# Kernel tuning notes

Hardware: AMD Instinct MI355X
Metric: run time of the kernel (lower is better)

## Reference

```python
import jax, jax.numpy as jnp
import numpy as np

N_NODES = 20000
N_EDGES = 320000
IN_F = 168
HID = 256


def gcn_conv(x, W, b, src, dst, ew, n_nodes):
    """PyG GCNConv: symmetric normalization with self-loops (fill 1.0).
    out = D^-1/2 (A + I) D^-1/2 X W^T + b, aggregated at dst (source_to_target).
    """
    xw = x @ W.T  # [N, F_out]
    # degree at target nodes, including self-loop weight 1.0
    deg = jax.ops.segment_sum(ew, dst, num_segments=n_nodes) + 1.0
    dinv = jnp.where(deg > 0, jax.lax.rsqrt(deg), 0.0)
    norm = dinv[src] * ew * dinv[dst]  # [E]
    agg = jax.ops.segment_sum(norm[:, None] * xw[src], dst, num_segments=n_nodes)
    # self-loop contribution: norm_ii = dinv[i]^2
    out = agg + (dinv * dinv)[:, None] * xw
    return out + b


def setup_inputs() -> dict:
    key = jax.random.key(0)
    k = jax.random.split(key, 8)
    x = jax.random.normal(k[0], (N_NODES, IN_F), dtype=jnp.float32)
    edge_index = jax.random.randint(k[1], (2, N_EDGES), 0, N_NODES, dtype=jnp.int64)
    edge_weight = jax.random.uniform(k[2], (N_EDGES,), dtype=jnp.float32)
    # GCN layer weights (PyG Linear: y = x W^T), plus per-layer bias
    s1 = 1.0 / np.sqrt(IN_F)
    s2 = 1.0 / np.sqrt(HID)
    W1 = jax.random.uniform(k[3], (HID, IN_F), minval=-s1, maxval=s1, dtype=jnp.float32)
    b1 = jnp.zeros((HID,), dtype=jnp.float32)
    W2 = jax.random.uniform(k[4], (HID, HID), minval=-s2, maxval=s2, dtype=jnp.float32)
    b2 = jnp.zeros((HID,), dtype=jnp.float32)
    return {"x": x, "edge_index": edge_index, "edge_weight": edge_weight,
            "W1": W1, "b1": b1, "W2": W2, "b2": b2}


def reference(x, edge_index, edge_weight, W1, b1, W2, b2):
    src, dst = edge_index[0], edge_index[1]
    h = gcn_conv(x, W1, b1, src, dst, edge_weight, N_NODES)
    h = jax.nn.relu(h)
    h = gcn_conv(h, W2, b2, src, dst, edge_weight, N_NODES)
    h = jax.nn.relu(h)
    return h
```

## Files before the change

kernel.cpp:

```cpp
#include <hip/hip_runtime.h>

#define N_NODES 20000
#define N_EDGES 320000
#define IN_F    168
#define HID     256
#define K1P     192
#define XS      192
#define NF4     42
#define X4      48

typedef __attribute__((ext_vector_type(8))) short bf16x8;
typedef __attribute__((ext_vector_type(4))) float f32x4;
typedef __attribute__((ext_vector_type(2))) float f32x2;

__device__ __forceinline__ short f2bf(float f) {
    union { float f; unsigned u; } v; v.f = f;
    unsigned r = v.u + 0x7FFFu + ((v.u >> 16) & 1u);
    return (short)(r >> 16);
}
__device__ __forceinline__ f32x2 bfp(unsigned u) {
    f32x2 r;
    r.x = __uint_as_float(u << 16);
    r.y = __uint_as_float(u & 0xFFFF0000u);
    return r;
}

__global__ void prep_all(const float* __restrict__ x, short* __restrict__ xb,
                         const float* __restrict__ W1, const float* __restrict__ W2,
                         short* __restrict__ w1b, short* __restrict__ w2b,
                         const int* __restrict__ ei, const float* __restrict__ ew,
                         float* __restrict__ deg, int* __restrict__ counts) {
    const int xTot  = N_NODES * X4;
    const int w1Tot = 256 * X4;
    const int w2Tot = 256 * 64;
    int i = blockIdx.x * 256 + threadIdx.x;
    if (i < xTot) {
        int n  = i / X4;
        int k4 = i - n * X4;
        short4 o;
        if (k4 < NF4) {
            float4 v = *(const float4*)(x + (size_t)n * IN_F + k4 * 4);
            o = make_short4(f2bf(v.x), f2bf(v.y), f2bf(v.z), f2bf(v.w));
        } else {
            o = make_short4(0, 0, 0, 0);
        }
        *(short4*)(xb + (size_t)n * XS + k4 * 4) = o;
        return;
    }
    i -= xTot;
    if (i < w1Tot) {
        int r  = i / X4;
        int k4 = i - r * X4;
        short4 o;
        if (k4 < NF4) {
            float4 v = *(const float4*)(W1 + (size_t)r * IN_F + k4 * 4);
            o = make_short4(f2bf(v.x), f2bf(v.y), f2bf(v.z), f2bf(v.w));
        } else {
            o = make_short4(0, 0, 0, 0);
        }
        *(short4*)(w1b + (size_t)r * K1P + k4 * 4) = o;
        return;
    }
    i -= w1Tot;
    if (i < w2Tot) {
        int r  = i >> 6;
        int c4 = i & 63;
        float4 v = *(const float4*)(W2 + (size_t)r * HID + c4 * 4);
        *(short4*)(w2b + (size_t)r * HID + c4 * 4) =
            make_short4(f2bf(v.x), f2bf(v.y), f2bf(v.z), f2bf(v.w));
        return;
    }
    i -= w2Tot;
    if (i < N_EDGES) {
        int d = ei[N_EDGES + i];
        atomicAdd(&deg[d], ew[i]);
        atomicAdd(&counts[d], 1);
    }
}


__global__ __launch_bounds__(1024) void scan_part(const int* __restrict__ counts,
                                                  int* __restrict__ offs,
                                                  int* __restrict__ bsum,
                                                  float* __restrict__ deg, int n) {
    int tid  = threadIdx.x;
    int lane = tid & 63;
    int wv   = tid >> 6;
    int i = blockIdx.x * 1024 + tid;
    if (i < n) deg[i] = rsqrtf(deg[i] + 1.0f);
    __shared__ int wsum[16];
    int v = (i < n) ? ((counts[i] + 7) & ~7) : 0;
    int incl = v;
    #pragma unroll
    for (int d = 1; d < 64; d <<= 1) {
        int t = __shfl_up(incl, d);
        if (lane >= d) incl += t;
    }
    if (lane == 63) wsum[wv] = incl;
    __syncthreads();
    if (wv == 0) {
        int w = (lane < 16) ? wsum[lane] : 0;
        int winc = w;
        #pragma unroll
        for (int d = 1; d < 16; d <<= 1) {
            int t = __shfl_up(winc, d);
            if (lane >= d) winc += t;
        }
        if (lane < 16) wsum[lane] = winc - w;
    }
    __syncthreads();
    if (i < n) offs[i] = wsum[wv] + incl - v;
    if (tid == 1023) bsum[blockIdx.x] = wsum[15] + incl;
}

__global__ __launch_bounds__(1024) void scan_add(const int* __restrict__ bsum,
                                                 int* __restrict__ offs, int n) {
    int i = blockIdx.x * 1024 + threadIdx.x;
    int add = 0;
    for (int b = 0; b < (int)blockIdx.x; ++b) add += bsum[b];
    if (i < n) offs[i] += add;
    if (i == n) offs[n] = add + bsum[blockIdx.x];
}

__global__ void scatter_edges(const int* __restrict__ ei, const float* __restrict__ ew,
                              const float* __restrict__ dinv, const int* __restrict__ offs,
                              const int* __restrict__ counts,
                              int* __restrict__ cursor, int2* __restrict__ er) {
    int t = blockIdx.x * 256 + threadIdx.x;
    if (t < N_EDGES) {
        int s = ei[t];
        int d = ei[N_EDGES + t];
        int pos = offs[d] + atomicAdd(&cursor[d], 1);
        float nm = dinv[s] * ew[t] * dinv[d];
        er[pos] = make_int2(s, __float_as_int(nm));
        return;
    }
    int n = t - N_EDGES;
    if (n < N_NODES) {
        int p   = offs[n] + counts[n];
        int end = offs[n + 1];
        for (; p < end; ++p) er[p] = make_int2(0, 0);
    }
}


__global__ __launch_bounds__(256) void agg_x(const short* __restrict__ xb,
                                             const float* __restrict__ dinv,
                                             const int* __restrict__ offs,
                                             const int2* __restrict__ er,
                                             short* __restrict__ ax) {
    int wave = threadIdx.x >> 6;
    int lane = threadIdx.x & 63;
    int n = blockIdx.x * 4 + wave;
    bool act = lane < NF4;
    int lo4 = act ? lane * 4 : 0;
    float di = dinv[n];
    float sw = di * di;
    uint2 sv = *(const uint2*)(xb + (size_t)n * XS + lo4);
    f32x2 a01 = bfp(sv.x) * sw;
    f32x2 a23 = bfp(sv.y) * sw;

    int p0 = offs[n], p1 = offs[n + 1];
    for (int p = p0; p < p1; p += 8) {
        const int4* e4 = (const int4*)(er + p);
        int4 eA = e4[0], eB = e4[1], eC = e4[2], eD = e4[3];
        uint2 r0 = *(const uint2*)(xb + (size_t)eA.x * XS + lo4);
        uint2 r1 = *(const uint2*)(xb + (size_t)eA.z * XS + lo4);
        uint2 r2 = *(const uint2*)(xb + (size_t)eB.x * XS + lo4);
        uint2 r3 = *(const uint2*)(xb + (size_t)eB.z * XS + lo4);
        uint2 r4 = *(const uint2*)(xb + (size_t)eC.x * XS + lo4);
        uint2 r5 = *(const uint2*)(xb + (size_t)eC.z * XS + lo4);
        uint2 r6 = *(const uint2*)(xb + (size_t)eD.x * XS + lo4);
        uint2 r7 = *(const uint2*)(xb + (size_t)eD.z * XS + lo4);
        float w0 = __int_as_float(eA.y), w1 = __int_as_float(eA.w);
        float w2 = __int_as_float(eB.y), w3 = __int_as_float(eB.w);
        float w4 = __int_as_float(eC.y), w5 = __int_as_float(eC.w);
        float w6 = __int_as_float(eD.y), w7 = __int_as_float(eD.w);
        a01 += bfp(r0.x) * w0; a23 += bfp(r0.y) * w0;
        a01 += bfp(r1.x) * w1; a23 += bfp(r1.y) * w1;
        a01 += bfp(r2.x) * w2; a23 += bfp(r2.y) * w2;
        a01 += bfp(r3.x) * w3; a23 += bfp(r3.y) * w3;
        a01 += bfp(r4.x) * w4; a23 += bfp(r4.y) * w4;
        a01 += bfp(r5.x) * w5; a23 += bfp(r5.y) * w5;
        a01 += bfp(r6.x) * w6; a23 += bfp(r6.y) * w6;
        a01 += bfp(r7.x) * w7; a23 += bfp(r7.y) * w7;
    }

    size_t base = (size_t)n * K1P + lane * 4;
    if (act) {
        *(short4*)&ax[base] = make_short4(f2bf(a01.x), f2bf(a01.y),
                                          f2bf(a23.x), f2bf(a23.y));
    } else if (lane < 48) {
        *(short4*)&ax[base] = make_short4(0, 0, 0, 0);
    }
}

__global__ __launch_bounds__(256) void agg_h(const short* __restrict__ h1h,
                                             const float* __restrict__ dinv,
                                             const int* __restrict__ offs,
                                             const int2* __restrict__ er,
                                             short* __restrict__ ah) {
    int wave = threadIdx.x >> 6;
    int lane = threadIdx.x & 63;
    int n = blockIdx.x * 4 + wave;
    int lo4 = lane * 4;
    float di = dinv[n];
    float sw = di * di;
    uint2 sv = *(const uint2*)(h1h + (size_t)n * HID + lo4);
    f32x2 a01 = bfp(sv.x) * sw;
    f32x2 a23 = bfp(sv.y) * sw;

    int p0 = offs[n], p1 = offs[n + 1];
    for (int p = p0; p < p1; p += 8) {
        const int4* e4 = (const int4*)(er + p);
        int4 eA = e4[0], eB = e4[1], eC = e4[2], eD = e4[3];
        uint2 r0 = *(const uint2*)(h1h + (size_t)eA.x * HID + lo4);
        uint2 r1 = *(const uint2*)(h1h + (size_t)eA.z * HID + lo4);
        uint2 r2 = *(const uint2*)(h1h + (size_t)eB.x * HID + lo4);
        uint2 r3 = *(const uint2*)(h1h + (size_t)eB.z * HID + lo4);
        uint2 r4 = *(const uint2*)(h1h + (size_t)eC.x * HID + lo4);
        uint2 r5 = *(const uint2*)(h1h + (size_t)eC.z * HID + lo4);
        uint2 r6 = *(const uint2*)(h1h + (size_t)eD.x * HID + lo4);
        uint2 r7 = *(const uint2*)(h1h + (size_t)eD.z * HID + lo4);
        float w0 = __int_as_float(eA.y), w1 = __int_as_float(eA.w);
        float w2 = __int_as_float(eB.y), w3 = __int_as_float(eB.w);
        float w4 = __int_as_float(eC.y), w5 = __int_as_float(eC.w);
        float w6 = __int_as_float(eD.y), w7 = __int_as_float(eD.w);
        a01 += bfp(r0.x) * w0; a23 += bfp(r0.y) * w0;
        a01 += bfp(r1.x) * w1; a23 += bfp(r1.y) * w1;
        a01 += bfp(r2.x) * w2; a23 += bfp(r2.y) * w2;
        a01 += bfp(r3.x) * w3; a23 += bfp(r3.y) * w3;
        a01 += bfp(r4.x) * w4; a23 += bfp(r4.y) * w4;
        a01 += bfp(r5.x) * w5; a23 += bfp(r5.y) * w5;
        a01 += bfp(r6.x) * w6; a23 += bfp(r6.y) * w6;
        a01 += bfp(r7.x) * w7; a23 += bfp(r7.y) * w7;
    }

    *(short4*)&ah[(size_t)n * HID + lo4] = make_short4(f2bf(a01.x), f2bf(a01.y),
                                                       f2bf(a23.x), f2bf(a23.y));
}


#define LDS_STRIDE 72

__global__ __launch_bounds__(256) void gemm_bf(const short* __restrict__ Ah,
                                               const short* __restrict__ Wh,
                                               const float* __restrict__ bias,
                                               float* __restrict__ Cf,
                                               short* __restrict__ Cbf,
                                               int M, int Ks, int nsteps, int mode) {
    __shared__ short sAh[64 * LDS_STRIDE];
    __shared__ short sWh[64 * LDS_STRIDE];

    const int idx   = blockIdx.x;
    const int group = idx >> 5;
    const int xcd   = idx & 7;
    const int slot  = (idx >> 3) & 3;
    const int mt    = group * 8 + xcd;
    const int mtiles = (M + 63) >> 6;
    if (mt >= mtiles) return;
    const int bm = mt * 64;
    const int bn = slot * 64;

    const int tid  = threadIdx.x;
    const int lane = tid & 63;
    const int wv   = tid >> 6;
    const int l16  = lane & 15;
    const int quad = lane >> 4;
    const int wm   = (wv & 1) * 32;
    const int wn   = (wv >> 1) * 32;

    const int srow = tid >> 2;
    const int sseg = (tid & 3) * 16;
    int arow = bm + srow; if (arow >= M) arow = M - 1;
    const short* gAh = Ah + (size_t)arow * Ks;
    const short* gWh = Wh + (size_t)(bn + srow) * Ks;
    const int lds_off = srow * LDS_STRIDE + sseg;

    f32x4 acc00 = {0,0,0,0}, acc01 = {0,0,0,0}, acc10 = {0,0,0,0}, acc11 = {0,0,0,0};

    int4 pah0 = *(const int4*)(gAh + sseg), pah1 = *(const int4*)(gAh + sseg + 8);
    int4 pwh0 = *(const int4*)(gWh + sseg), pwh1 = *(const int4*)(gWh + sseg + 8);

    for (int ks = 0; ks < nsteps; ++ks) {
        *(int4*)&sAh[lds_off] = pah0; *(int4*)&sAh[lds_off + 8] = pah1;
        *(int4*)&sWh[lds_off] = pwh0; *(int4*)&sWh[lds_off + 8] = pwh1;
        __syncthreads();
        if (ks + 1 < nsteps) {
            int o = (ks + 1) * 64 + sseg;
            pah0 = *(const int4*)(gAh + o); pah1 = *(const int4*)(gAh + o + 8);
            pwh0 = *(const int4*)(gWh + o); pwh1 = *(const int4*)(gWh + o + 8);
        }
        #pragma unroll
        for (int o = 0; o < 2; ++o) {
            const int a0 = (wm + l16) * LDS_STRIDE + o * 32 + quad * 8;
            const int a1 = a0 + 16 * LDS_STRIDE;
            const int w0 = (wn + l16) * LDS_STRIDE + o * 32 + quad * 8;
            const int w1 = w0 + 16 * LDS_STRIDE;
            bf16x8 ah0 = *(const bf16x8*)&sAh[a0];
            bf16x8 ah1 = *(const bf16x8*)&sAh[a1];
            bf16x8 wh0 = *(const bf16x8*)&sWh[w0];
            bf16x8 wh1 = *(const bf16x8*)&sWh[w1];
            acc00 = __builtin_amdgcn_mfma_f32_16x16x32_bf16(ah0, wh0, acc00, 0, 0, 0);
            acc01 = __builtin_amdgcn_mfma_f32_16x16x32_bf16(ah0, wh1, acc01, 0, 0, 0);
            acc10 = __builtin_amdgcn_mfma_f32_16x16x32_bf16(ah1, wh0, acc10, 0, 0, 0);
            acc11 = __builtin_amdgcn_mfma_f32_16x16x32_bf16(ah1, wh1, acc11, 0, 0, 0);
        }
        __syncthreads();
    }

    const int colb = bn + wn + l16;
    const int rowb = bm + wm + quad * 4;
    const float b0 = bias[colb];
    const float b1 = bias[colb + 16];
    #pragma unroll
    for (int r = 0; r < 4; ++r) {
        int row = rowb + r;
        if (row < M) {
            float v0 = acc00[r] + b0; v0 = v0 > 0.f ? v0 : 0.f;
            float v1 = acc01[r] + b1; v1 = v1 > 0.f ? v1 : 0.f;
            if (mode == 0) {
                Cbf[(size_t)row * HID + colb]      = f2bf(v0);
                Cbf[(size_t)row * HID + colb + 16] = f2bf(v1);
            } else {
                Cf[(size_t)row * HID + colb]      = v0;
                Cf[(size_t)row * HID + colb + 16] = v1;
            }
        }
        int row2 = row + 16;
        if (row2 < M) {
            float v0 = acc10[r] + b0; v0 = v0 > 0.f ? v0 : 0.f;
            float v1 = acc11[r] + b1; v1 = v1 > 0.f ? v1 : 0.f;
            if (mode == 0) {
                Cbf[(size_t)row2 * HID + colb]      = f2bf(v0);
                Cbf[(size_t)row2 * HID + colb + 16] = f2bf(v1);
            } else {
                Cf[(size_t)row2 * HID + colb]      = v0;
                Cf[(size_t)row2 * HID + colb + 16] = v1;
            }
        }
    }
}


extern "C" void kernel_launch(void* const* d_in, const int* in_sizes, int n_in,
                              void* d_out, int out_size, void* d_ws, size_t ws_size,
                              hipStream_t stream) {
    const float* x  = (const float*)d_in[0];
    const int*   ei = (const int*)d_in[1];
    const float* ew = (const float*)d_in[2];
    const float* W1 = (const float*)d_in[3];
    const float* b1 = (const float*)d_in[4];
    const float* W2 = (const float*)d_in[5];
    const float* b2 = (const float*)d_in[6];
    float* out = (float*)d_out;

    char* ws = (char*)d_ws;
    float* deg      = (float*)(ws);
    int*   counts   = (int*)(ws + 80000);
    int*   cursor   = (int*)(ws + 160000);
    int*   offs     = (int*)(ws + 240000);
    int*   bsum     = (int*)(ws + 320016);
    int2*  er       = (int2*)(ws + 320144);
    short* ax       = (short*)(ws + 4160144);
    short* ah       = (short*)(ws + 4160144);
    short* h1h      = (short*)(ws + 14400144);
    short* w1b      = (short*)(ws + 24640144);
    short* w2b      = (short*)(ws + 24738448);
    short* xb       = (short*)(ws + 24869520);

    hipMemsetAsync(d_ws, 0, 320144, stream);

    const int prep_tot = N_NODES * X4 + 256 * X4 + 256 * 64 + N_EDGES;
    prep_all<<<(prep_tot + 255) / 256, 256, 0, stream>>>(
        x, xb, W1, W2, w1b, w2b, ei, ew, deg, counts);
    scan_part<<<20, 1024, 0, stream>>>(counts, offs, bsum, deg, N_NODES);
    scan_add<<<20, 1024, 0, stream>>>(bsum, offs, N_NODES);
    const int sc_blocks = (N_EDGES + N_NODES + 255) / 256;
    scatter_edges<<<sc_blocks, 256, 0, stream>>>(ei, ew, deg, offs, counts, cursor, er);

    const int mtiles = (N_NODES + 63) / 64;
    const int gemm_grid = ((mtiles + 7) / 8) * 32;
    agg_x<<<N_NODES / 4, 256, 0, stream>>>(xb, deg, offs, er, ax);
    gemm_bf<<<gemm_grid, 256, 0, stream>>>(ax, w1b, b1, nullptr, h1h,
                                           N_NODES, K1P, 3, 0);
    agg_h<<<N_NODES / 4, 256, 0, stream>>>(h1h, deg, offs, er, ah);
    gemm_bf<<<gemm_grid, 256, 0, stream>>>(ah, w2b, b2, out, nullptr,
                                           N_NODES, HID, 4, 1);
}
```

Measured before the change: 200.1 us.

## Fuse aggregation with GEMM per layer and merge scan into one kernel

Each layer's neighbor aggregation now writes its 64-row tile straight into shared memory and the same block runs the MFMA GEMM over all four column slots. This removes the global round trip for the aggregated activations and two kernel launches. The two-kernel prefix scan is replaced by a single 1024-thread block in which each thread scans 20 entries. That block also resets the cursor array, so the memset shrinks. The cost is much lower parallelism: only 313 blocks each doing 64 rows of serial gather, plus a single-block scan.

```diff
diff --git a/kernel.cpp b/kernel.cpp
--- a/kernel.cpp
+++ b/kernel.cpp
@@ -8,6 +8,9 @@
 #define XS      192
 #define NF4     42
 #define X4      48
+#define ASTR1   200
+#define ASTR2   264
+#define WSTR    72
 
 typedef __attribute__((ext_vector_type(8))) short bf16x8;
 typedef __attribute__((ext_vector_type(4))) float f32x4;
@@ -78,19 +81,33 @@
     }
 }
 
-
-__global__ __launch_bounds__(1024) void scan_part(const int* __restrict__ counts,
-                                                  int* __restrict__ offs,
-                                                  int* __restrict__ bsum,
-                                                  float* __restrict__ deg, int n) {
-    int tid  = threadIdx.x;
-    int lane = tid & 63;
-    int wv   = tid >> 6;
-    int i = blockIdx.x * 1024 + tid;
-    if (i < n) deg[i] = rsqrtf(deg[i] + 1.0f);
+__global__ __launch_bounds__(1024) void scan1(const int* __restrict__ counts,
+                                              int* __restrict__ offs,
+                                              float* __restrict__ deg,
+                                              int* __restrict__ cursor) {
+    const int tid  = threadIdx.x;
+    const int lane = tid & 63;
+    const int wv   = tid >> 6;
     __shared__ int wsum[16];
-    int v = (i < n) ? ((counts[i] + 7) & ~7) : 0;
-    int incl = v;
+
+    const int base = tid * 20;
+    int loc[20];
+    int s = 0;
+    #pragma unroll
+    for (int j = 0; j < 20; ++j) {
+        int i = base + j;
+        int c = (i < N_NODES) ? ((counts[i] + 7) & ~7) : 0;
+        loc[j] = s; s += c;
+    }
+    #pragma unroll
+    for (int j = 0; j < 20; ++j) {
+        int i = base + j;
+        if (i < N_NODES) {
+            deg[i] = rsqrtf(deg[i] + 1.0f);
+            cursor[i] = 0;
+        }
+    }
+    int incl = s;
     #pragma unroll
     for (int d = 1; d < 64; d <<= 1) {
         int t = __shfl_up(incl, d);
@@ -109,17 +126,13 @@
         if (lane < 16) wsum[lane] = winc - w;
     }
     __syncthreads();
-    if (i < n) offs[i] = wsum[wv] + incl - v;
-    if (tid == 1023) bsum[blockIdx.x] = wsum[15] + incl;
-}
-
-__global__ __launch_bounds__(1024) void scan_add(const int* __restrict__ bsum,
-                                                 int* __restrict__ offs, int n) {
-    int i = blockIdx.x * 1024 + threadIdx.x;
-    int add = 0;
-    for (int b = 0; b < (int)blockIdx.x; ++b) add += bsum[b];
-    if (i < n) offs[i] += add;
-    if (i == n) offs[n] = add + bsum[blockIdx.x];
+    int excl = wsum[wv] + incl - s;
+    #pragma unroll
+    for (int j = 0; j < 20; ++j) {
+        int i = base + j;
+        if (i < N_NODES) offs[i] = excl + loc[j];
+    }
+    if (tid == 1023) offs[N_NODES] = excl + s;
 }
 
 __global__ void scatter_edges(const int* __restrict__ ei, const float* __restrict__ ew,
@@ -143,200 +156,245 @@
     }
 }
 
-
-__global__ __launch_bounds__(256) void agg_x(const short* __restrict__ xb,
-                                             const float* __restrict__ dinv,
-                                             const int* __restrict__ offs,
-                                             const int2* __restrict__ er,
-                                             short* __restrict__ ax) {
-    int wave = threadIdx.x >> 6;
-    int lane = threadIdx.x & 63;
-    int n = blockIdx.x * 4 + wave;
-    bool act = lane < NF4;
-    int lo4 = act ? lane * 4 : 0;
-    float di = dinv[n];
-    float sw = di * di;
-    uint2 sv = *(const uint2*)(xb + (size_t)n * XS + lo4);
-    f32x2 a01 = bfp(sv.x) * sw;
-    f32x2 a23 = bfp(sv.y) * sw;
-
-    int p0 = offs[n], p1 = offs[n + 1];
-    for (int p = p0; p < p1; p += 8) {
-        const int4* e4 = (const int4*)(er + p);
-        int4 eA = e4[0], eB = e4[1], eC = e4[2], eD = e4[3];
-        uint2 r0 = *(const uint2*)(xb + (size_t)eA.x * XS + lo4);
-        uint2 r1 = *(const uint2*)(xb + (size_t)eA.z * XS + lo4);
-        uint2 r2 = *(const uint2*)(xb + (size_t)eB.x * XS + lo4);
-        uint2 r3 = *(const uint2*)(xb + (size_t)eB.z * XS + lo4);
-        uint2 r4 = *(const uint2*)(xb + (size_t)eC.x * XS + lo4);
-        uint2 r5 = *(const uint2*)(xb + (size_t)eC.z * XS + lo4);
-        uint2 r6 = *(const uint2*)(xb + (size_t)eD.x * XS + lo4);
-        uint2 r7 = *(const uint2*)(xb + (size_t)eD.z * XS + lo4);
-        float w0 = __int_as_float(eA.y), w1 = __int_as_float(eA.w);
-        float w2 = __int_as_float(eB.y), w3 = __int_as_float(eB.w);
-        float w4 = __int_as_float(eC.y), w5 = __int_as_float(eC.w);
-        float w6 = __int_as_float(eD.y), w7 = __int_as_float(eD.w);
-        a01 += bfp(r0.x) * w0; a23 += bfp(r0.y) * w0;
-        a01 += bfp(r1.x) * w1; a23 += bfp(r1.y) * w1;
-        a01 += bfp(r2.x) * w2; a23 += bfp(r2.y) * w2;
-        a01 += bfp(r3.x) * w3; a23 += bfp(r3.y) * w3;
-        a01 += bfp(r4.x) * w4; a23 += bfp(r4.y) * w4;
-        a01 += bfp(r5.x) * w5; a23 += bfp(r5.y) * w5;
-        a01 += bfp(r6.x) * w6; a23 += bfp(r6.y) * w6;
-        a01 += bfp(r7.x) * w7; a23 += bfp(r7.y) * w7;
-    }
-
-    size_t base = (size_t)n * K1P + lane * 4;
-    if (act) {
-        *(short4*)&ax[base] = make_short4(f2bf(a01.x), f2bf(a01.y),
-                                          f2bf(a23.x), f2bf(a23.y));
-    } else if (lane < 48) {
-        *(short4*)&ax[base] = make_short4(0, 0, 0, 0);
-    }
-}
-
-__global__ __launch_bounds__(256) void agg_h(const short* __restrict__ h1h,
-                                             const float* __restrict__ dinv,
-                                             const int* __restrict__ offs,
-                                             const int2* __restrict__ er,
-                                             short* __restrict__ ah) {
-    int wave = threadIdx.x >> 6;
-    int lane = threadIdx.x & 63;
-    int n = blockIdx.x * 4 + wave;
-    int lo4 = lane * 4;
-    float di = dinv[n];
-    float sw = di * di;
-    uint2 sv = *(const uint2*)(h1h + (size_t)n * HID + lo4);
-    f32x2 a01 = bfp(sv.x) * sw;
-    f32x2 a23 = bfp(sv.y) * sw;
-
-    int p0 = offs[n], p1 = offs[n + 1];
-    for (int p = p0; p < p1; p += 8) {
-        const int4* e4 = (const int4*)(er + p);
-        int4 eA = e4[0], eB = e4[1], eC = e4[2], eD = e4[3];
-        uint2 r0 = *(const uint2*)(h1h + (size_t)eA.x * HID + lo4);
-        uint2 r1 = *(const uint2*)(h1h + (size_t)eA.z * HID + lo4);
-        uint2 r2 = *(const uint2*)(h1h + (size_t)eB.x * HID + lo4);
-        uint2 r3 = *(const uint2*)(h1h + (size_t)eB.z * HID + lo4);
-        uint2 r4 = *(const uint2*)(h1h + (size_t)eC.x * HID + lo4);
-        uint2 r5 = *(const uint2*)(h1h + (size_t)eC.z * HID + lo4);
-        uint2 r6 = *(const uint2*)(h1h + (size_t)eD.x * HID + lo4);
-        uint2 r7 = *(const uint2*)(h1h + (size_t)eD.z * HID + lo4);
-        float w0 = __int_as_float(eA.y), w1 = __int_as_float(eA.w);
-        float w2 = __int_as_float(eB.y), w3 = __int_as_float(eB.w);
-        float w4 = __int_as_float(eC.y), w5 = __int_as_float(eC.w);
-        float w6 = __int_as_float(eD.y), w7 = __int_as_float(eD.w);
-        a01 += bfp(r0.x) * w0; a23 += bfp(r0.y) * w0;
-        a01 += bfp(r1.x) * w1; a23 += bfp(r1.y) * w1;
-        a01 += bfp(r2.x) * w2; a23 += bfp(r2.y) * w2;
-        a01 += bfp(r3.x) * w3; a23 += bfp(r3.y) * w3;
-        a01 += bfp(r4.x) * w4; a23 += bfp(r4.y) * w4;
-        a01 += bfp(r5.x) * w5; a23 += bfp(r5.y) * w5;
-        a01 += bfp(r6.x) * w6; a23 += bfp(r6.y) * w6;
-        a01 += bfp(r7.x) * w7; a23 += bfp(r7.y) * w7;
-    }
-
-    *(short4*)&ah[(size_t)n * HID + lo4] = make_short4(f2bf(a01.x), f2bf(a01.y),
-                                                       f2bf(a23.x), f2bf(a23.y));
-}
-
-
-#define LDS_STRIDE 72
-
-__global__ __launch_bounds__(256) void gemm_bf(const short* __restrict__ Ah,
-                                               const short* __restrict__ Wh,
-                                               const float* __restrict__ bias,
-                                               float* __restrict__ Cf,
-                                               short* __restrict__ Cbf,
-                                               int M, int Ks, int nsteps, int mode) {
-    __shared__ short sAh[64 * LDS_STRIDE];
-    __shared__ short sWh[64 * LDS_STRIDE];
-
-    const int idx   = blockIdx.x;
-    const int group = idx >> 5;
-    const int xcd   = idx & 7;
-    const int slot  = (idx >> 3) & 3;
-    const int mt    = group * 8 + xcd;
-    const int mtiles = (M + 63) >> 6;
-    if (mt >= mtiles) return;
-    const int bm = mt * 64;
-    const int bn = slot * 64;
+__global__ __launch_bounds__(256) void fused1(
+    const short* __restrict__ xb, const float* __restrict__ dinv,
+    const int* __restrict__ offs, const int2* __restrict__ er,
+    const short* __restrict__ w1b, const float* __restrict__ b1,
+    short* __restrict__ h1h)
+{
+    __shared__ short sA[64 * ASTR1];
+    __shared__ short sW[64 * WSTR];
 
     const int tid  = threadIdx.x;
+    const int wave = tid >> 6;
     const int lane = tid & 63;
-    const int wv   = tid >> 6;
+    const int bm   = blockIdx.x * 64;
+
+    {
+        bool act = lane < NF4;
+        int lo4 = act ? lane * 4 : 0;
+        for (int i = 0; i < 16; ++i) {
+            int r = wave * 16 + i;
+            int n = bm + r;
+            if (n < N_NODES) {
+                float di = dinv[n];
+                float sw = di * di;
+                uint2 sv = *(const uint2*)(xb + (size_t)n * XS + lo4);
+                f32x2 a01 = bfp(sv.x) * sw;
+                f32x2 a23 = bfp(sv.y) * sw;
+                int p1v = offs[n + 1];
+                for (int p = offs[n]; p < p1v; p += 8) {
+                    const int4* e4 = (const int4*)(er + p);
+                    int4 eA = e4[0], eB = e4[1], eC = e4[2], eD = e4[3];
+                    uint2 r0 = *(const uint2*)(xb + (size_t)eA.x * XS + lo4);
+                    uint2 r1 = *(const uint2*)(xb + (size_t)eA.z * XS + lo4);
+                    uint2 r2 = *(const uint2*)(xb + (size_t)eB.x * XS + lo4);
+                    uint2 r3 = *(const uint2*)(xb + (size_t)eB.z * XS + lo4);
+                    uint2 r4 = *(const uint2*)(xb + (size_t)eC.x * XS + lo4);
+                    uint2 r5 = *(const uint2*)(xb + (size_t)eC.z * XS + lo4);
+                    uint2 r6 = *(const uint2*)(xb + (size_t)eD.x * XS + lo4);
+                    uint2 r7 = *(const uint2*)(xb + (size_t)eD.z * XS + lo4);
+                    float w0 = __int_as_float(eA.y), w1 = __int_as_float(eA.w);
+                    float w2 = __int_as_float(eB.y), w3 = __int_as_float(eB.w);
+                    float w4 = __int_as_float(eC.y), w5 = __int_as_float(eC.w);
+                    float w6 = __int_as_float(eD.y), w7 = __int_as_float(eD.w);
+                    a01 += bfp(r0.x) * w0; a23 += bfp(r0.y) * w0;
+                    a01 += bfp(r1.x) * w1; a23 += bfp(r1.y) * w1;
+                    a01 += bfp(r2.x) * w2; a23 += bfp(r2.y) * w2;
+                    a01 += bfp(r3.x) * w3; a23 += bfp(r3.y) * w3;
+                    a01 += bfp(r4.x) * w4; a23 += bfp(r4.y) * w4;
+                    a01 += bfp(r5.x) * w5; a23 += bfp(r5.y) * w5;
+                    a01 += bfp(r6.x) * w6; a23 += bfp(r6.y) * w6;
+                    a01 += bfp(r7.x) * w7; a23 += bfp(r7.y) * w7;
+                }
+                if (act) {
+                    *(short4*)&sA[r * ASTR1 + lane * 4] =
+                        make_short4(f2bf(a01.x), f2bf(a01.y), f2bf(a23.x), f2bf(a23.y));
+                } else if (lane < 48) {
+                    *(short4*)&sA[r * ASTR1 + lane * 4] = make_short4(0, 0, 0, 0);
+                }
+            } else {
+                if (lane < 48)
+                    *(short4*)&sA[r * ASTR1 + lane * 4] = make_short4(0, 0, 0, 0);
+            }
+        }
+    }
+    __syncthreads();
+
     const int l16  = lane & 15;
     const int quad = lane >> 4;
-    const int wm   = (wv & 1) * 32;
-    const int wn   = (wv >> 1) * 32;
-
+    const int wm   = (wave & 1) * 32;
+    const int wn   = (wave >> 1) * 32;
     const int srow = tid >> 2;
     const int sseg = (tid & 3) * 16;
-    int arow = bm + srow; if (arow >= M) arow = M - 1;
-    const short* gAh = Ah + (size_t)arow * Ks;
-    const short* gWh = Wh + (size_t)(bn + srow) * Ks;
-    const int lds_off = srow * LDS_STRIDE + sseg;
-
-    f32x4 acc00 = {0,0,0,0}, acc01 = {0,0,0,0}, acc10 = {0,0,0,0}, acc11 = {0,0,0,0};
-
-    int4 pah0 = *(const int4*)(gAh + sseg), pah1 = *(const int4*)(gAh + sseg + 8);
-    int4 pwh0 = *(const int4*)(gWh + sseg), pwh1 = *(const int4*)(gWh + sseg + 8);
-
-    for (int ks = 0; ks < nsteps; ++ks) {
-        *(int4*)&sAh[lds_off] = pah0; *(int4*)&sAh[lds_off + 8] = pah1;
-        *(int4*)&sWh[lds_off] = pwh0; *(int4*)&sWh[lds_off + 8] = pwh1;
-        __syncthreads();
-        if (ks + 1 < nsteps) {
-            int o = (ks + 1) * 64 + sseg;
-            pah0 = *(const int4*)(gAh + o); pah1 = *(const int4*)(gAh + o + 8);
-            pwh0 = *(const int4*)(gWh + o); pwh1 = *(const int4*)(gWh + o + 8);
-        }
+    const int lds_off = srow * WSTR + sseg;
+    const int M = N_NODES;
+
+    for (int slot = 0; slot < 4; ++slot) {
+        const int bn = slot * 64;
+        const short* gW = w1b + (size_t)(bn + srow) * K1P;
+        f32x4 acc00 = {0,0,0,0}, acc01 = {0,0,0,0}, acc10 = {0,0,0,0}, acc11 = {0,0,0,0};
+        int4 pw0 = *(const int4*)(gW + sseg), pw1 = *(const int4*)(gW + sseg + 8);
+        for (int ks = 0; ks < 3; ++ks) {
+            *(int4*)&sW[lds_off] = pw0; *(int4*)&sW[lds_off + 8] = pw1;
+            __syncthreads();
+            if (ks < 2) {
+                int o = (ks + 1) * 64 + sseg;
+                pw0 = *(const int4*)(gW + o); pw1 = *(const int4*)(gW + o + 8);
+            }
+            #pragma unroll
+            for (int o = 0; o < 2; ++o) {
+                const int ak = ks * 64 + o * 32 + quad * 8;
+                bf16x8 ah0 = *(const bf16x8*)&sA[(wm + l16) * ASTR1 + ak];
+                bf16x8 ah1 = *(const bf16x8*)&sA[(wm + 16 + l16) * ASTR1 + ak];
+                const int w0 = (wn + l16) * WSTR + o * 32 + quad * 8;
+                bf16x8 wh0 = *(const bf16x8*)&sW[w0];
+                bf16x8 wh1 = *(const bf16x8*)&sW[w0 + 16 * WSTR];
+                acc00 = __builtin_amdgcn_mfma_f32_16x16x32_bf16(ah0, wh0, acc00, 0, 0, 0);
+                acc01 = __builtin_amdgcn_mfma_f32_16x16x32_bf16(ah0, wh1, acc01, 0, 0, 0);
+                acc10 = __builtin_amdgcn_mfma_f32_16x16x32_bf16(ah1, wh0, acc10, 0, 0, 0);
+                acc11 = __builtin_amdgcn_mfma_f32_16x16x32_bf16(ah1, wh1, acc11, 0, 0, 0);
+            }
+            __syncthreads();
+        }
+        const int colb = bn + wn + l16;
+        const int rowb = bm + wm + quad * 4;
+        const float bb0 = b1[colb];
+        const float bb1 = b1[colb + 16];
         #pragma unroll
-        for (int o = 0; o < 2; ++o) {
-            const int a0 = (wm + l16) * LDS_STRIDE + o * 32 + quad * 8;
-            const int a1 = a0 + 16 * LDS_STRIDE;
-            const int w0 = (wn + l16) * LDS_STRIDE + o * 32 + quad * 8;
-            const int w1 = w0 + 16 * LDS_STRIDE;
-            bf16x8 ah0 = *(const bf16x8*)&sAh[a0];
-            bf16x8 ah1 = *(const bf16x8*)&sAh[a1];
-            bf16x8 wh0 = *(const bf16x8*)&sWh[w0];
-            bf16x8 wh1 = *(const bf16x8*)&sWh[w1];
-            acc00 = __builtin_amdgcn_mfma_f32_16x16x32_bf16(ah0, wh0, acc00, 0, 0, 0);
-            acc01 = __builtin_amdgcn_mfma_f32_16x16x32_bf16(ah0, wh1, acc01, 0, 0, 0);
-            acc10 = __builtin_amdgcn_mfma_f32_16x16x32_bf16(ah1, wh0, acc10, 0, 0, 0);
-            acc11 = __builtin_amdgcn_mfma_f32_16x16x32_bf16(ah1, wh1, acc11, 0, 0, 0);
-        }
-        __syncthreads();
-    }
-
-    const int colb = bn + wn + l16;
-    const int rowb = bm + wm + quad * 4;
-    const float b0 = bias[colb];
-    const float b1 = bias[colb + 16];
-    #pragma unroll
-    for (int r = 0; r < 4; ++r) {
-        int row = rowb + r;
-        if (row < M) {
-            float v0 = acc00[r] + b0; v0 = v0 > 0.f ? v0 : 0.f;
-            float v1 = acc01[r] + b1; v1 = v1 > 0.f ? v1 : 0.f;
-            if (mode == 0) {
-                Cbf[(size_t)row * HID + colb]      = f2bf(v0);
-                Cbf[(size_t)row * HID + colb + 16] = f2bf(v1);
+        for (int r = 0; r < 4; ++r) {
+            int row = rowb + r;
+            if (row < M) {
+                float v0 = acc00[r] + bb0; v0 = v0 > 0.f ? v0 : 0.f;
+                float v1 = acc01[r] + bb1; v1 = v1 > 0.f ? v1 : 0.f;
+                h1h[(size_t)row * HID + colb]      = f2bf(v0);
+                h1h[(size_t)row * HID + colb + 16] = f2bf(v1);
+            }
+            int row2 = row + 16;
+            if (row2 < M) {
+                float v0 = acc10[r] + bb0; v0 = v0 > 0.f ? v0 : 0.f;
+                float v1 = acc11[r] + bb1; v1 = v1 > 0.f ? v1 : 0.f;
+                h1h[(size_t)row2 * HID + colb]      = f2bf(v0);
+                h1h[(size_t)row2 * HID + colb + 16] = f2bf(v1);
+            }
+        }
+    }
+}
+
+__global__ __launch_bounds__(256) void fused2(
+    const short* __restrict__ h1h, const float* __restrict__ dinv,
+    const int* __restrict__ offs, const int2* __restrict__ er,
+    const short* __restrict__ w2b, const float* __restrict__ b2,
+    float* __restrict__ out)
+{
+    __shared__ short sA[64 * ASTR2];
+    __shared__ short sW[64 * WSTR];
+
+    const int tid  = threadIdx.x;
+    const int wave = tid >> 6;
+    const int lane = tid & 63;
+    const int bm   = blockIdx.x * 64;
+
+    {
+        int lo4 = lane * 4;
+        for (int i = 0; i < 16; ++i) {
+            int r = wave * 16 + i;
+            int n = bm + r;
+            if (n < N_NODES) {
+                float di = dinv[n];
+                float sw = di * di;
+                uint2 sv = *(const uint2*)(h1h + (size_t)n * HID + lo4);
+                f32x2 a01 = bfp(sv.x) * sw;
+                f32x2 a23 = bfp(sv.y) * sw;
+                int p1v = offs[n + 1];
+                for (int p = offs[n]; p < p1v; p += 8) {
+                    const int4* e4 = (const int4*)(er + p);
+                    int4 eA = e4[0], eB = e4[1], eC = e4[2], eD = e4[3];
+                    uint2 r0 = *(const uint2*)(h1h + (size_t)eA.x * HID + lo4);
+                    uint2 r1 = *(const uint2*)(h1h + (size_t)eA.z * HID + lo4);
+                    uint2 r2 = *(const uint2*)(h1h + (size_t)eB.x * HID + lo4);
+                    uint2 r3 = *(const uint2*)(h1h + (size_t)eB.z * HID + lo4);
+                    uint2 r4 = *(const uint2*)(h1h + (size_t)eC.x * HID + lo4);
+                    uint2 r5 = *(const uint2*)(h1h + (size_t)eC.z * HID + lo4);
+                    uint2 r6 = *(const uint2*)(h1h + (size_t)eD.x * HID + lo4);
+                    uint2 r7 = *(const uint2*)(h1h + (size_t)eD.z * HID + lo4);
+                    float w0 = __int_as_float(eA.y), w1 = __int_as_float(eA.w);
+                    float w2 = __int_as_float(eB.y), w3 = __int_as_float(eB.w);
+                    float w4 = __int_as_float(eC.y), w5 = __int_as_float(eC.w);
+                    float w6 = __int_as_float(eD.y), w7 = __int_as_float(eD.w);
+                    a01 += bfp(r0.x) * w0; a23 += bfp(r0.y) * w0;
+                    a01 += bfp(r1.x) * w1; a23 += bfp(r1.y) * w1;
+                    a01 += bfp(r2.x) * w2; a23 += bfp(r2.y) * w2;
+                    a01 += bfp(r3.x) * w3; a23 += bfp(r3.y) * w3;
+                    a01 += bfp(r4.x) * w4; a23 += bfp(r4.y) * w4;
+                    a01 += bfp(r5.x) * w5; a23 += bfp(r5.y) * w5;
+                    a01 += bfp(r6.x) * w6; a23 += bfp(r6.y) * w6;
+                    a01 += bfp(r7.x) * w7; a23 += bfp(r7.y) * w7;
+                }
+                *(short4*)&sA[r * ASTR2 + lo4] =
+                    make_short4(f2bf(a01.x), f2bf(a01.y), f2bf(a23.x), f2bf(a23.y));
             } else {
-                Cf[(size_t)row * HID + colb]      = v0;
-                Cf[(size_t)row * HID + colb + 16] = v1;
-            }
-        }
-        int row2 = row + 16;
-        if (row2 < M) {
-            float v0 = acc10[r] + b0; v0 = v0 > 0.f ? v0 : 0.f;
-            float v1 = acc11[r] + b1; v1 = v1 > 0.f ? v1 : 0.f;
-            if (mode == 0) {
-                Cbf[(size_t)row2 * HID + colb]      = f2bf(v0);
-                Cbf[(size_t)row2 * HID + colb + 16] = f2bf(v1);
-            } else {
-                Cf[(size_t)row2 * HID + colb]      = v0;
-                Cf[(size_t)row2 * HID + colb + 16] = v1;
+                *(short4*)&sA[r * ASTR2 + lo4] = make_short4(0, 0, 0, 0);
+            }
+        }
+    }
+    __syncthreads();
+
+    const int l16  = lane & 15;
+    const int quad = lane >> 4;
+    const int wm   = (wave & 1) * 32;
+    const int wn   = (wave >> 1) * 32;
+    const int srow = tid >> 2;
+    const int sseg = (tid & 3) * 16;
+    const int lds_off = srow * WSTR + sseg;
+    const int M = N_NODES;
+
+    for (int slot = 0; slot < 4; ++slot) {
+        const int bn = slot * 64;
+        const short* gW = w2b + (size_t)(bn + srow) * HID;
+        f32x4 acc00 = {0,0,0,0}, acc01 = {0,0,0,0}, acc10 = {0,0,0,0}, acc11 = {0,0,0,0};
+        int4 pw0 = *(const int4*)(gW + sseg), pw1 = *(const int4*)(gW + sseg + 8);
+        for (int ks = 0; ks < 4; ++ks) {
+            *(int4*)&sW[lds_off] = pw0; *(int4*)&sW[lds_off + 8] = pw1;
+            __syncthreads();
+            if (ks < 3) {
+                int o = (ks + 1) * 64 + sseg;
+                pw0 = *(const int4*)(gW + o); pw1 = *(const int4*)(gW + o + 8);
+            }
+            #pragma unroll
+            for (int o = 0; o < 2; ++o) {
+                const int ak = ks * 64 + o * 32 + quad * 8;
+                bf16x8 ah0 = *(const bf16x8*)&sA[(wm + l16) * ASTR2 + ak];
+                bf16x8 ah1 = *(const bf16x8*)&sA[(wm + 16 + l16) * ASTR2 + ak];
+                const int w0 = (wn + l16) * WSTR + o * 32 + quad * 8;
+                bf16x8 wh0 = *(const bf16x8*)&sW[w0];
+                bf16x8 wh1 = *(const bf16x8*)&sW[w0 + 16 * WSTR];
+                acc00 = __builtin_amdgcn_mfma_f32_16x16x32_bf16(ah0, wh0, acc00, 0, 0, 0);
+                acc01 = __builtin_amdgcn_mfma_f32_16x16x32_bf16(ah0, wh1, acc01, 0, 0, 0);
+                acc10 = __builtin_amdgcn_mfma_f32_16x16x32_bf16(ah1, wh0, acc10, 0, 0, 0);
+                acc11 = __builtin_amdgcn_mfma_f32_16x16x32_bf16(ah1, wh1, acc11, 0, 0, 0);
+            }
+            __syncthreads();
+        }
+        const int colb = bn + wn + l16;
+        const int rowb = bm + wm + quad * 4;
+        const float bb0 = b2[colb];
+        const float bb1 = b2[colb + 16];
+        #pragma unroll
+        for (int r = 0; r < 4; ++r) {
+            int row = rowb + r;
+            if (row < M) {
+                float v0 = acc00[r] + bb0; v0 = v0 > 0.f ? v0 : 0.f;
+                float v1 = acc01[r] + bb1; v1 = v1 > 0.f ? v1 : 0.f;
+                out[(size_t)row * HID + colb]      = v0;
+                out[(size_t)row * HID + colb + 16] = v1;
+            }
+            int row2 = row + 16;
+            if (row2 < M) {
+                float v0 = acc10[r] + bb0; v0 = v0 > 0.f ? v0 : 0.f;
+                float v1 = acc11[r] + bb1; v1 = v1 > 0.f ? v1 : 0.f;
+                out[(size_t)row2 * HID + colb]      = v0;
+                out[(size_t)row2 * HID + colb + 16] = v1;
             }
         }
     }
@@ -360,31 +418,22 @@
     int*   counts   = (int*)(ws + 80000);
     int*   cursor   = (int*)(ws + 160000);
     int*   offs     = (int*)(ws + 240000);
-    int*   bsum     = (int*)(ws + 320016);
     int2*  er       = (int2*)(ws + 320144);
-    short* ax       = (short*)(ws + 4160144);
-    short* ah       = (short*)(ws + 4160144);
     short* h1h      = (short*)(ws + 14400144);
     short* w1b      = (short*)(ws + 24640144);
     short* w2b      = (short*)(ws + 24738448);
     short* xb       = (short*)(ws + 24869520);
 
-    hipMemsetAsync(d_ws, 0, 320144, stream);
+    hipMemsetAsync(d_ws, 0, 160000, stream);
 
     const int prep_tot = N_NODES * X4 + 256 * X4 + 256 * 64 + N_EDGES;
     prep_all<<<(prep_tot + 255) / 256, 256, 0, stream>>>(
         x, xb, W1, W2, w1b, w2b, ei, ew, deg, counts);
-    scan_part<<<20, 1024, 0, stream>>>(counts, offs, bsum, deg, N_NODES);
-    scan_add<<<20, 1024, 0, stream>>>(bsum, offs, N_NODES);
+    scan1<<<1, 1024, 0, stream>>>(counts, offs, deg, cursor);
     const int sc_blocks = (N_EDGES + N_NODES + 255) / 256;
     scatter_edges<<<sc_blocks, 256, 0, stream>>>(ei, ew, deg, offs, counts, cursor, er);
 
     const int mtiles = (N_NODES + 63) / 64;
-    const int gemm_grid = ((mtiles + 7) / 8) * 32;
-    agg_x<<<N_NODES / 4, 256, 0, stream>>>(xb, deg, offs, er, ax);
-    gemm_bf<<<gemm_grid, 256, 0, stream>>>(ax, w1b, b1, nullptr, h1h,
-                                           N_NODES, K1P, 3, 0);
-    agg_h<<<N_NODES / 4, 256, 0, stream>>>(h1h, deg, offs, er, ah);
-    gemm_bf<<<gemm_grid, 256, 0, stream>>>(ah, w2b, b2, out, nullptr,
-                                           N_NODES, HID, 4, 1);
-}
+    fused1<<<mtiles, 256, 0, stream>>>(xb, deg, offs, er, w1b, b1, h1h);
+    fused2<<<mtiles, 256, 0, stream>>>(h1h, deg, offs, er, w2b, b2, out);
+}
```

Result: slower. 290.3 us (+45.0%).

## Split aggregation across edge groups and feature slices; single-block scan

Applied to the files above, without the earlier changes.

The aggregation kernels now split each node's work. Each wave covers a quarter of the feature columns, and the four 16-lane groups each take two of the eight padded edges per step, with partial sums combined by cross-lane shuffles. The grid grows fourfold and block indices are remapped so that slices of the same node land on related XCDs. The two-kernel scan is replaced by one 1024-thread block in which each thread handles 20 counts and also resets the cursor, so the memset shrinks. This trades more blocks and shuffle reductions for more memory-level parallelism and fewer launches.

```diff
diff --git a/kernel.cpp b/kernel.cpp
--- a/kernel.cpp
+++ b/kernel.cpp
@@ -78,19 +78,33 @@
     }
 }
 
-
-__global__ __launch_bounds__(1024) void scan_part(const int* __restrict__ counts,
-                                                  int* __restrict__ offs,
-                                                  int* __restrict__ bsum,
-                                                  float* __restrict__ deg, int n) {
-    int tid  = threadIdx.x;
-    int lane = tid & 63;
-    int wv   = tid >> 6;
-    int i = blockIdx.x * 1024 + tid;
-    if (i < n) deg[i] = rsqrtf(deg[i] + 1.0f);
+__global__ __launch_bounds__(1024) void scan1(const int* __restrict__ counts,
+                                              int* __restrict__ offs,
+                                              float* __restrict__ deg,
+                                              int* __restrict__ cursor) {
+    const int tid  = threadIdx.x;
+    const int lane = tid & 63;
+    const int wv   = tid >> 6;
     __shared__ int wsum[16];
-    int v = (i < n) ? ((counts[i] + 7) & ~7) : 0;
-    int incl = v;
+
+    const int base = tid * 20;
+    int loc[20];
+    int s = 0;
+    #pragma unroll
+    for (int j = 0; j < 20; ++j) {
+        int i = base + j;
+        int c = (i < N_NODES) ? ((counts[i] + 7) & ~7) : 0;
+        loc[j] = s; s += c;
+    }
+    #pragma unroll
+    for (int j = 0; j < 20; ++j) {
+        int i = base + j;
+        if (i < N_NODES) {
+            deg[i] = rsqrtf(deg[i] + 1.0f);
+            cursor[i] = 0;
+        }
+    }
+    int incl = s;
     #pragma unroll
     for (int d = 1; d < 64; d <<= 1) {
         int t = __shfl_up(incl, d);
@@ -109,17 +123,13 @@
         if (lane < 16) wsum[lane] = winc - w;
     }
     __syncthreads();
-    if (i < n) offs[i] = wsum[wv] + incl - v;
-    if (tid == 1023) bsum[blockIdx.x] = wsum[15] + incl;
-}
-
-__global__ __launch_bounds__(1024) void scan_add(const int* __restrict__ bsum,
-                                                 int* __restrict__ offs, int n) {
-    int i = blockIdx.x * 1024 + threadIdx.x;
-    int add = 0;
-    for (int b = 0; b < (int)blockIdx.x; ++b) add += bsum[b];
-    if (i < n) offs[i] += add;
-    if (i == n) offs[n] = add + bsum[blockIdx.x];
+    int excl = wsum[wv] + incl - s;
+    #pragma unroll
+    for (int j = 0; j < 20; ++j) {
+        int i = base + j;
+        if (i < N_NODES) offs[i] = excl + loc[j];
+    }
+    if (tid == 1023) offs[N_NODES] = excl + s;
 }
 
 __global__ void scatter_edges(const int* __restrict__ ei, const float* __restrict__ ew,
@@ -149,49 +159,44 @@
                                              const int* __restrict__ offs,
                                              const int2* __restrict__ er,
                                              short* __restrict__ ax) {
-    int wave = threadIdx.x >> 6;
-    int lane = threadIdx.x & 63;
-    int n = blockIdx.x * 4 + wave;
-    bool act = lane < NF4;
-    int lo4 = act ? lane * 4 : 0;
-    float di = dinv[n];
-    float sw = di * di;
-    uint2 sv = *(const uint2*)(xb + (size_t)n * XS + lo4);
-    f32x2 a01 = bfp(sv.x) * sw;
-    f32x2 a23 = bfp(sv.y) * sw;
-
-    int p0 = offs[n], p1 = offs[n + 1];
-    for (int p = p0; p < p1; p += 8) {
-        const int4* e4 = (const int4*)(er + p);
-        int4 eA = e4[0], eB = e4[1], eC = e4[2], eD = e4[3];
-        uint2 r0 = *(const uint2*)(xb + (size_t)eA.x * XS + lo4);
-        uint2 r1 = *(const uint2*)(xb + (size_t)eA.z * XS + lo4);
-        uint2 r2 = *(const uint2*)(xb + (size_t)eB.x * XS + lo4);
-        uint2 r3 = *(const uint2*)(xb + (size_t)eB.z * XS + lo4);
-        uint2 r4 = *(const uint2*)(xb + (size_t)eC.x * XS + lo4);
-        uint2 r5 = *(const uint2*)(xb + (size_t)eC.z * XS + lo4);
-        uint2 r6 = *(const uint2*)(xb + (size_t)eD.x * XS + lo4);
-        uint2 r7 = *(const uint2*)(xb + (size_t)eD.z * XS + lo4);
-        float w0 = __int_as_float(eA.y), w1 = __int_as_float(eA.w);
-        float w2 = __int_as_float(eB.y), w3 = __int_as_float(eB.w);
-        float w4 = __int_as_float(eC.y), w5 = __int_as_float(eC.w);
-        float w6 = __int_as_float(eD.y), w7 = __int_as_float(eD.w);
+    const int bid  = blockIdx.x;
+    const int s    = (bid & 7) >> 1;
+    const int sub  = (bid >> 3) * 2 + (bid & 1);
+    const int wave = threadIdx.x >> 6;
+    const int lane = threadIdx.x & 63;
+    const int g    = lane >> 4;
+    const int l16  = lane & 15;
+    const int n    = sub * 4 + wave;
+    const bool act = l16 < 12;
+    const int fo   = act ? (s * 48 + l16 * 4) : 0;
+
+    f32x2 a01 = {0.f, 0.f}, a23 = {0.f, 0.f};
+    if (g == 0) {
+        float di = dinv[n];
+        float sw = di * di;
+        uint2 sv = *(const uint2*)(xb + (size_t)n * XS + fo);
+        a01 = bfp(sv.x) * sw;
+        a23 = bfp(sv.y) * sw;
+    }
+    const int p1 = offs[n + 1];
+    for (int p = offs[n]; p < p1; p += 8) {
+        int4 e = ((const int4*)(er + p))[g];
+        uint2 r0 = *(const uint2*)(xb + (size_t)e.x * XS + fo);
+        uint2 r1 = *(const uint2*)(xb + (size_t)e.z * XS + fo);
+        float w0 = __int_as_float(e.y), w1 = __int_as_float(e.w);
         a01 += bfp(r0.x) * w0; a23 += bfp(r0.y) * w0;
         a01 += bfp(r1.x) * w1; a23 += bfp(r1.y) * w1;
-        a01 += bfp(r2.x) * w2; a23 += bfp(r2.y) * w2;
-        a01 += bfp(r3.x) * w3; a23 += bfp(r3.y) * w3;
-        a01 += bfp(r4.x) * w4; a23 += bfp(r4.y) * w4;
-        a01 += bfp(r5.x) * w5; a23 += bfp(r5.y) * w5;
-        a01 += bfp(r6.x) * w6; a23 += bfp(r6.y) * w6;
-        a01 += bfp(r7.x) * w7; a23 += bfp(r7.y) * w7;
-    }
-
-    size_t base = (size_t)n * K1P + lane * 4;
-    if (act) {
-        *(short4*)&ax[base] = make_short4(f2bf(a01.x), f2bf(a01.y),
-                                          f2bf(a23.x), f2bf(a23.y));
-    } else if (lane < 48) {
-        *(short4*)&ax[base] = make_short4(0, 0, 0, 0);
+    }
+    #pragma unroll
+    for (int off = 16; off < 64; off <<= 1) {
+        a01.x += __shfl_xor(a01.x, off);
+        a01.y += __shfl_xor(a01.y, off);
+        a23.x += __shfl_xor(a23.x, off);
+        a23.y += __shfl_xor(a23.y, off);
+    }
+    if (g == 0 && act) {
+        *(short4*)&ax[(size_t)n * K1P + fo] =
+            make_short4(f2bf(a01.x), f2bf(a01.y), f2bf(a23.x), f2bf(a23.y));
     }
 }
 
@@ -200,46 +205,45 @@
                                              const int* __restrict__ offs,
                                              const int2* __restrict__ er,
                                              short* __restrict__ ah) {
-    int wave = threadIdx.x >> 6;
-    int lane = threadIdx.x & 63;
-    int n = blockIdx.x * 4 + wave;
-    int lo4 = lane * 4;
-    float di = dinv[n];
-    float sw = di * di;
-    uint2 sv = *(const uint2*)(h1h + (size_t)n * HID + lo4);
-    f32x2 a01 = bfp(sv.x) * sw;
-    f32x2 a23 = bfp(sv.y) * sw;
-
-    int p0 = offs[n], p1 = offs[n + 1];
-    for (int p = p0; p < p1; p += 8) {
-        const int4* e4 = (const int4*)(er + p);
-        int4 eA = e4[0], eB = e4[1], eC = e4[2], eD = e4[3];
-        uint2 r0 = *(const uint2*)(h1h + (size_t)eA.x * HID + lo4);
-        uint2 r1 = *(const uint2*)(h1h + (size_t)eA.z * HID + lo4);
-        uint2 r2 = *(const uint2*)(h1h + (size_t)eB.x * HID + lo4);
-        uint2 r3 = *(const uint2*)(h1h + (size_t)eB.z * HID + lo4);
-        uint2 r4 = *(const uint2*)(h1h + (size_t)eC.x * HID + lo4);
-        uint2 r5 = *(const uint2*)(h1h + (size_t)eC.z * HID + lo4);
-        uint2 r6 = *(const uint2*)(h1h + (size_t)eD.x * HID + lo4);
-        uint2 r7 = *(const uint2*)(h1h + (size_t)eD.z * HID + lo4);
-        float w0 = __int_as_float(eA.y), w1 = __int_as_float(eA.w);
-        float w2 = __int_as_float(eB.y), w3 = __int_as_float(eB.w);
-        float w4 = __int_as_float(eC.y), w5 = __int_as_float(eC.w);
-        float w6 = __int_as_float(eD.y), w7 = __int_as_float(eD.w);
+    const int bid  = blockIdx.x;
+    const int s    = (bid & 7) >> 1;
+    const int sub  = (bid >> 3) * 2 + (bid & 1);
+    const int wave = threadIdx.x >> 6;
+    const int lane = threadIdx.x & 63;
+    const int g    = lane >> 4;
+    const int l16  = lane & 15;
+    const int n    = sub * 4 + wave;
+    const int fo   = s * 64 + l16 * 4;
+
+    f32x2 a01 = {0.f, 0.f}, a23 = {0.f, 0.f};
+    if (g == 0) {
+        float di = dinv[n];
+        float sw = di * di;
+        uint2 sv = *(const uint2*)(h1h + (size_t)n * HID + fo);
+        a01 = bfp(sv.x) * sw;
+        a23 = bfp(sv.y) * sw;
+    }
+    const int p1 = offs[n + 1];
+    for (int p = offs[n]; p < p1; p += 8) {
+        int4 e = ((const int4*)(er + p))[g];
+        uint2 r0 = *(const uint2*)(h1h + (size_t)e.x * HID + fo);
+        uint2 r1 = *(const uint2*)(h1h + (size_t)e.z * HID + fo);
+        float w0 = __int_as_float(e.y), w1 = __int_as_float(e.w);
         a01 += bfp(r0.x) * w0; a23 += bfp(r0.y) * w0;
         a01 += bfp(r1.x) * w1; a23 += bfp(r1.y) * w1;
-        a01 += bfp(r2.x) * w2; a23 += bfp(r2.y) * w2;
-        a01 += bfp(r3.x) * w3; a23 += bfp(r3.y) * w3;
-        a01 += bfp(r4.x) * w4; a23 += bfp(r4.y) * w4;
-        a01 += bfp(r5.x) * w5; a23 += bfp(r5.y) * w5;
-        a01 += bfp(r6.x) * w6; a23 += bfp(r6.y) * w6;
-        a01 += bfp(r7.x) * w7; a23 += bfp(r7.y) * w7;
-    }
-
-    *(short4*)&ah[(size_t)n * HID + lo4] = make_short4(f2bf(a01.x), f2bf(a01.y),
-                                                       f2bf(a23.x), f2bf(a23.y));
-}
-
+    }
+    #pragma unroll
+    for (int off = 16; off < 64; off <<= 1) {
+        a01.x += __shfl_xor(a01.x, off);
+        a01.y += __shfl_xor(a01.y, off);
+        a23.x += __shfl_xor(a23.x, off);
+        a23.y += __shfl_xor(a23.y, off);
+    }
+    if (g == 0) {
+        *(short4*)&ah[(size_t)n * HID + fo] =
+            make_short4(f2bf(a01.x), f2bf(a01.y), f2bf(a23.x), f2bf(a23.y));
+    }
+}
 
 #define LDS_STRIDE 72
 
@@ -360,7 +364,6 @@
     int*   counts   = (int*)(ws + 80000);
     int*   cursor   = (int*)(ws + 160000);
     int*   offs     = (int*)(ws + 240000);
-    int*   bsum     = (int*)(ws + 320016);
     int2*  er       = (int2*)(ws + 320144);
     short* ax       = (short*)(ws + 4160144);
     short* ah       = (short*)(ws + 4160144);
@@ -369,22 +372,23 @@
     short* w2b      = (short*)(ws + 24738448);
     short* xb       = (short*)(ws + 24869520);
 
-    hipMemsetAsync(d_ws, 0, 320144, stream);
+    hipMemsetAsync(d_ws, 0, 160000, stream);
 
     const int prep_tot = N_NODES * X4 + 256 * X4 + 256 * 64 + N_EDGES;
     prep_all<<<(prep_tot + 255) / 256, 256, 0, stream>>>(
         x, xb, W1, W2, w1b, w2b, ei, ew, deg, counts);
-    scan_part<<<20, 1024, 0, stream>>>(counts, offs, bsum, deg, N_NODES);
-    scan_add<<<20, 1024, 0, stream>>>(bsum, offs, N_NODES);
+    scan1<<<1, 1024, 0, stream>>>(counts, offs, deg, cursor);
     const int sc_blocks = (N_EDGES + N_NODES + 255) / 256;
     scatter_edges<<<sc_blocks, 256, 0, stream>>>(ei, ew, deg, offs, counts, cursor, er);
 
     const int mtiles = (N_NODES + 63) / 64;
     const int gemm_grid = ((mtiles + 7) / 8) * 32;
-    agg_x<<<N_NODES / 4, 256, 0, stream>>>(xb, deg, offs, er, ax);
+    const int agg_grid = N_NODES;
+
+    agg_x<<<agg_grid, 256, 0, stream>>>(xb, deg, offs, er, ax);
     gemm_bf<<<gemm_grid, 256, 0, stream>>>(ax, w1b, b1, nullptr, h1h,
                                            N_NODES, K1P, 3, 0);
-    agg_h<<<N_NODES / 4, 256, 0, stream>>>(h1h, deg, offs, er, ah);
+    agg_h<<<agg_grid, 256, 0, stream>>>(h1h, deg, offs, er, ah);
     gemm_bf<<<gemm_grid, 256, 0, stream>>>(ah, w2b, b2, out, nullptr,
                                            N_NODES, HID, 4, 1);
 }
```

New measurement: 272.2 us. +36.0%, slower.
